# Optimization experiments

Hardware: AMD Instinct MI355X
Metric: run time of the kernel (lower is better)

## Reference

```python
import jax, jax.numpy as jnp
import numpy as np

B, S, H = 4, 2048, 768
NUM_POS = B * (S // 4)  # fixed count of positive clc_label entries (2048, even)
NEG_BIG = -1000000000.0


def setup_inputs() -> dict:
    key = jax.random.key(0)
    k1, k2, k3, k4, k5 = jax.random.split(key, 5)
    encoded_states = jax.random.normal(k1, (B, S, H), dtype=jnp.float32)
    # sorted cell-ids -> contiguous segments for the equality mask
    indicator = jnp.sort(jax.random.randint(k2, (B, S), 0, 256, dtype=jnp.int32), axis=-1)
    # clc_label: first S//4 positions per row are positive targets (class ids in [1,S)),
    # last S//2 positions are -1 (attendable keys), rest 0 (ignored)
    pos_labels = jax.random.randint(k3, (B, S // 4), 1, S, dtype=jnp.int32)
    clc_label = jnp.zeros((B, S), dtype=jnp.int32)
    clc_label = clc_label.at[:, : S // 4].set(pos_labels)
    clc_label = clc_label.at[:, S // 2:].set(-1)
    # uniform_linear params (torch Linear: y = x @ W.T + b)
    W = jax.random.normal(k4, (H, H), dtype=jnp.float32) / np.sqrt(H)
    b = jax.random.normal(k5, (H,), dtype=jnp.float32) * 0.01
    return {"encoded_states": encoded_states, "W": W, "b": b,
            "indicator": indicator, "clc_label": clc_label}


def _ce(logits, labels):
    # mean cross entropy; all labels are > 0 here so ignore_index=0 never triggers
    logp = jax.nn.log_softmax(logits, axis=-1)
    return -jnp.take_along_axis(logp, labels[:, None], axis=1).mean()


def reference(encoded_states, W, b, indicator, clc_label):
    # indicator-equality mask matmul == within-segment sum (the segment-reduce emulation)
    seg_mask = (indicator[:, :, None] == indicator[:, None, :]).astype(encoded_states.dtype)  # [B,S,S]
    agg = jnp.einsum("bij,bjh->bih", seg_mask, encoded_states)  # [B,S,H]
    # Q and K use the SAME linear on the same input -> compute once
    proj = jnp.tanh(agg @ W.T + b)  # [B,S,H]
    scores = jnp.einsum("bih,bjh->bij", proj, proj)  # [B,S,S]
    # attend only to positions where clc_label < 0
    allow = (clc_label < 0)[:, None, :]  # [B,1,S]
    scores = scores + jnp.where(allow, 0.0, NEG_BIG).astype(scores.dtype)
    flat = scores.reshape(-1, S)          # [B*S, S]
    labels = clc_label.reshape(-1)        # [B*S]
    pos_idx = jnp.nonzero(labels > 0, size=NUM_POS)[0]  # row-major order == torch bool-indexing
    logits = flat[pos_idx]                # [NUM_POS, S]
    labs = labels[pos_idx]                # [NUM_POS]
    sep_logits, sep_labels = logits[0::2], labs[0::2]
    tok_logits, tok_labels = logits[1::2], labs[1::2]
    sep_loss = _ce(sep_logits, sep_labels)
    tok_loss = _ce(tok_logits, tok_labels)
    sep_correct = jnp.sum((jnp.argmax(sep_logits, axis=-1).astype(jnp.int32) == sep_labels).astype(jnp.float32))
    tok_correct = jnp.sum((jnp.argmax(tok_logits, axis=-1).astype(jnp.int32) == tok_labels).astype(jnp.float32))
    sep_count = jnp.asarray(sep_logits.shape[0] + 1e-6, dtype=jnp.float32)
    tok_count = jnp.asarray(tok_logits.shape[0] + 1e-6, dtype=jnp.float32)
    return ((sep_loss, sep_correct, sep_count), (tok_loss, tok_correct, tok_count))
```

## Files before the change

kernel.cpp:

```cpp
#include <hip/hip_runtime.h>
#include <math.h>
#include <limits.h>

#define BB 4
#define SS 2048
#define HH 768
#define MAXSEG 256
#define NUM_POS (BB*(SS/4))
#define NEG_BIG -1000000000.0f

typedef _Float16 f16x8 __attribute__((ext_vector_type(8)));
typedef _Float16 f16x4 __attribute__((ext_vector_type(4)));
typedef float    f32x4 __attribute__((ext_vector_type(4)));

__global__ __launch_bounds__(256) void k_scanW(
    const int* __restrict__ ind, const int* __restrict__ clc,
    const float* __restrict__ W, _Float16* __restrict__ Wh,
    int* __restrict__ seg_id, int* __restrict__ seg_start,
    int* __restrict__ nseg, int* __restrict__ pos_local, int* __restrict__ pos_cnt,
    int* __restrict__ allowCnt, int* __restrict__ firstAllow)
{
  int t = threadIdx.x;
  if (blockIdx.x >= BB) {
    int idx = (blockIdx.x - BB)*256 + t;
    float4 v = ((const float4*)W)[idx];
    f16x4 h;
    h[0] = (_Float16)v.x; h[1] = (_Float16)v.y;
    h[2] = (_Float16)v.z; h[3] = (_Float16)v.w;
    *(f16x4*)(Wh + (size_t)idx*4) = h;
    return;
  }
  int b = blockIdx.x;
  int lane = t & 63, wid = t >> 6;
  __shared__ int sInd[SS];
  __shared__ int sWave[4];
  __shared__ int sAC[MAXSEG];
  __shared__ int sFA[MAXSEG];
  for (int i = t; i < SS; i += 256) sInd[i] = ind[b*SS + i];
  sAC[t] = 0; sFA[t] = INT_MAX;
  __syncthreads();

  int i0 = t * 8;
  int f[8], cv[8];
  int lsum = 0;
  #pragma unroll
  for (int u = 0; u < 8; u++) {
    int i = i0 + u;
    f[u] = (i == 0) ? 0 : (sInd[i] != sInd[i-1]);
    cv[u] = clc[b*SS + i];
    lsum += f[u];
  }
  int x = lsum;
  #pragma unroll
  for (int off = 1; off < 64; off <<= 1) {
    int v = __shfl_up(x, off, 64);
    if (lane >= off) x += v;
  }
  if (lane == 63) sWave[wid] = x;
  __syncthreads();
  int base = 0;
  for (int w = 0; w < wid; w++) base += sWave[w];
  int run = base + x - lsum;
  int rid[8];
  #pragma unroll
  for (int u = 0; u < 8; u++) {
    int i = i0 + u;
    run += f[u];
    rid[u] = run;
    seg_id[b*SS + i] = run;
    if (f[u] || i == 0) seg_start[b*(MAXSEG+1) + run] = i;
  }
  if (t == 255) { nseg[b] = run + 1; seg_start[b*(MAXSEG+1) + run + 1] = SS; }

  #pragma unroll
  for (int u = 0; u < 8; u++) {
    if (cv[u] < 0) {
      atomicAdd(&sAC[rid[u]], 1);
      atomicMin(&sFA[rid[u]], i0 + u);
    }
  }
  __syncthreads();
  allowCnt[b*MAXSEG + t]   = sAC[t];
  firstAllow[b*MAXSEG + t] = sFA[t];

  int psum = 0;
  int p[8];
  #pragma unroll
  for (int u = 0; u < 8; u++) { p[u] = (cv[u] > 0) ? 1 : 0; psum += p[u]; }
  x = psum;
  #pragma unroll
  for (int off = 1; off < 64; off <<= 1) {
    int v = __shfl_up(x, off, 64);
    if (lane >= off) x += v;
  }
  __syncthreads();
  if (lane == 63) sWave[wid] = x;
  __syncthreads();
  base = 0;
  for (int w = 0; w < wid; w++) base += sWave[w];
  int rank = base + x - psum;
  #pragma unroll
  for (int u = 0; u < 8; u++) {
    if (p[u]) { pos_local[b*SS + rank] = i0 + u; rank++; }
  }
  if (t == 255) pos_cnt[b] = rank;
}

__global__ __launch_bounds__(256) void k_segsum(
    const float* __restrict__ es,
    const int* __restrict__ seg_start, const int* __restrict__ nseg,
    _Float16* __restrict__ segsum_h)
{
  int blk = blockIdx.x, t = threadIdx.x;
  int b = blk >> 8, s = blk & 255;
  _Float16* o = segsum_h + ((size_t)b*MAXSEG + s)*HH;
  if (s >= nseg[b]) {
    o[t] = (_Float16)0.f; o[t+256] = (_Float16)0.f; o[t+512] = (_Float16)0.f;
    return;
  }
  int st = seg_start[b*(MAXSEG+1) + s];
  int en = seg_start[b*(MAXSEG+1) + s + 1];
  const float* base = es + (size_t)b*SS*HH;
  float a0 = 0.f, a1 = 0.f, a2 = 0.f;
  float b0 = 0.f, b1 = 0.f, b2 = 0.f;
  float c0 = 0.f, c1 = 0.f, c2 = 0.f;
  float d0 = 0.f, d1 = 0.f, d2 = 0.f;
  int i = st;
  for (; i + 4 <= en; i += 4) {
    const float* r0 = base + (size_t)i*HH;
    const float* r1 = r0 + HH;
    const float* r2 = r1 + HH;
    const float* r3 = r2 + HH;
    a0 += r0[t]; a1 += r0[t+256]; a2 += r0[t+512];
    b0 += r1[t]; b1 += r1[t+256]; b2 += r1[t+512];
    c0 += r2[t]; c1 += r2[t+256]; c2 += r2[t+512];
    d0 += r3[t]; d1 += r3[t+256]; d2 += r3[t+512];
  }
  for (; i < en; i++) {
    const float* r = base + (size_t)i*HH;
    a0 += r[t]; a1 += r[t+256]; a2 += r[t+512];
  }
  o[t]     = (_Float16)((a0 + b0) + (c0 + d0));
  o[t+256] = (_Float16)((a1 + b1) + (c1 + d1));
  o[t+512] = (_Float16)((a2 + b2) + (c2 + d2));
}

__global__ __launch_bounds__(256) void k_gemmU(
    const _Float16* __restrict__ Ah, const _Float16* __restrict__ Wh,
    const float* __restrict__ bias, _Float16* __restrict__ Uh)
{
  int tid = threadIdx.x;
  int w = tid >> 6, lane = tid & 63;
  int tile = blockIdx.x*4 + w;
  int tm = tile / 24, tn = tile % 24;
  int rb = tm*32, cb = tn*32;
  int m0 = lane & 15, quad = lane >> 4;
  const _Float16* A0 = Ah + (size_t)(rb + m0)*HH + quad*8;
  const _Float16* A1 = A0 + (size_t)16*HH;
  const _Float16* B0 = Wh + (size_t)(cb + m0)*HH + quad*8;
  const _Float16* B1 = B0 + (size_t)16*HH;
  f32x4 acc00 = {0.f,0.f,0.f,0.f}, acc01 = {0.f,0.f,0.f,0.f};
  f32x4 acc10 = {0.f,0.f,0.f,0.f}, acc11 = {0.f,0.f,0.f,0.f};
  #pragma unroll 4
  for (int k0 = 0; k0 < HH; k0 += 32) {
    f16x8 a0 = *(const f16x8*)(A0 + k0);
    f16x8 a1 = *(const f16x8*)(A1 + k0);
    f16x8 b0 = *(const f16x8*)(B0 + k0);
    f16x8 b1 = *(const f16x8*)(B1 + k0);
    acc00 = __builtin_amdgcn_mfma_f32_16x16x32_f16(a0, b0, acc00, 0, 0, 0);
    acc01 = __builtin_amdgcn_mfma_f32_16x16x32_f16(a0, b1, acc01, 0, 0, 0);
    acc10 = __builtin_amdgcn_mfma_f32_16x16x32_f16(a1, b0, acc10, 0, 0, 0);
    acc11 = __builtin_amdgcn_mfma_f32_16x16x32_f16(a1, b1, acc11, 0, 0, 0);
  }
  float bc0 = bias[cb + m0], bc1 = bias[cb + 16 + m0];
  int r0 = rb + quad*4;
  #pragma unroll
  for (int i = 0; i < 4; i++) {
    Uh[(size_t)(r0+i)*HH    + cb + m0]      = (_Float16)tanhf(acc00[i] + bc0);
    Uh[(size_t)(r0+i)*HH    + cb + 16 + m0] = (_Float16)tanhf(acc01[i] + bc1);
    Uh[(size_t)(r0+16+i)*HH + cb + m0]      = (_Float16)tanhf(acc10[i] + bc0);
    Uh[(size_t)(r0+16+i)*HH + cb + 16 + m0] = (_Float16)tanhf(acc11[i] + bc1);
  }
}

__global__ __launch_bounds__(256) void k_gramlse(
    const _Float16* __restrict__ Uh, const int* __restrict__ allowCnt,
    const int* __restrict__ firstAllow, const int* __restrict__ nseg,
    float* __restrict__ G, float* __restrict__ lse, int* __restrict__ amax)
{
  __shared__ float sG[16][257];
  int t = threadIdx.x;
  int lane = t & 63, w = t >> 6;
  int blk = blockIdx.x;
  int b = blk >> 4;
  int rb = (blk & 15) * 16;
  int m0 = lane & 15, quad = lane >> 4;
  const _Float16* Ub = Uh + (size_t)b*MAXSEG*HH;
  const _Float16* A0 = Ub + (size_t)(rb + m0)*HH + quad*8;
  int cb0 = w * 64;
  const _Float16* B0 = Ub + (size_t)(cb0      + m0)*HH + quad*8;
  const _Float16* B1 = Ub + (size_t)(cb0 + 16 + m0)*HH + quad*8;
  const _Float16* B2 = Ub + (size_t)(cb0 + 32 + m0)*HH + quad*8;
  const _Float16* B3 = Ub + (size_t)(cb0 + 48 + m0)*HH + quad*8;
  f32x4 acc0 = {0.f,0.f,0.f,0.f}, acc1 = {0.f,0.f,0.f,0.f};
  f32x4 acc2 = {0.f,0.f,0.f,0.f}, acc3 = {0.f,0.f,0.f,0.f};
  #pragma unroll 4
  for (int k0 = 0; k0 < HH; k0 += 32) {
    f16x8 a  = *(const f16x8*)(A0 + k0);
    f16x8 q0 = *(const f16x8*)(B0 + k0);
    f16x8 q1 = *(const f16x8*)(B1 + k0);
    f16x8 q2 = *(const f16x8*)(B2 + k0);
    f16x8 q3 = *(const f16x8*)(B3 + k0);
    acc0 = __builtin_amdgcn_mfma_f32_16x16x32_f16(a, q0, acc0, 0, 0, 0);
    acc1 = __builtin_amdgcn_mfma_f32_16x16x32_f16(a, q1, acc1, 0, 0, 0);
    acc2 = __builtin_amdgcn_mfma_f32_16x16x32_f16(a, q2, acc2, 0, 0, 0);
    acc3 = __builtin_amdgcn_mfma_f32_16x16x32_f16(a, q3, acc3, 0, 0, 0);
  }
  float* Gb = G + (size_t)b*MAXSEG*MAXSEG;
  int r0 = quad*4;
  #pragma unroll
  for (int i = 0; i < 4; i++) {
    int rl = r0 + i;
    sG[rl][cb0      + m0] = acc0[i];
    sG[rl][cb0 + 16 + m0] = acc1[i];
    sG[rl][cb0 + 32 + m0] = acc2[i];
    sG[rl][cb0 + 48 + m0] = acc3[i];
    float* gr = Gb + (size_t)(rb + rl)*MAXSEG;
    gr[cb0      + m0] = acc0[i];
    gr[cb0 + 16 + m0] = acc1[i];
    gr[cb0 + 32 + m0] = acc2[i];
    gr[cb0 + 48 + m0] = acc3[i];
  }
  __syncthreads();

  const int* ac = allowCnt + b*MAXSEG;
  const int* fa = firstAllow + b*MAXSEG;
  int ns = nseg[b];
  #pragma unroll
  for (int j = 0; j < 4; j++) {
    int rl = w*4 + j;
    int si = rb + rl;
    if (si >= ns) continue;
    float gv[4]; int av[4], fv[4];
    #pragma unroll
    for (int q = 0; q < 4; q++) {
      int s = lane + 64*q;
      gv[q] = sG[rl][s]; av[q] = ac[s]; fv[q] = fa[s];
    }
    float m = -INFINITY;
    #pragma unroll
    for (int q = 0; q < 4; q++) if (av[q] > 0) m = fmaxf(m, gv[q]);
    #pragma unroll
    for (int off = 32; off > 0; off >>= 1) m = fmaxf(m, __shfl_xor(m, off, 64));
    float s = 0.f;
    #pragma unroll
    for (int q = 0; q < 4; q++) if (av[q] > 0) s += (float)av[q] * expf(gv[q] - m);
    #pragma unroll
    for (int off = 32; off > 0; off >>= 1) s += __shfl_xor(s, off, 64);
    float bv = -INFINITY; int bi = INT_MAX;
    #pragma unroll
    for (int q = 0; q < 4; q++) {
      if (av[q] > 0 && (gv[q] > bv || (gv[q] == bv && fv[q] < bi))) { bv = gv[q]; bi = fv[q]; }
    }
    #pragma unroll
    for (int off = 32; off > 0; off >>= 1) {
      float ov = __shfl_xor(bv, off, 64);
      int   oi = __shfl_xor(bi, off, 64);
      if (ov > bv || (ov == bv && oi < bi)) { bv = ov; bi = oi; }
    }
    if (lane == 0) {
      lse[b*MAXSEG + si]  = m + logf(s);
      amax[b*MAXSEG + si] = bi;
    }
  }
}

__global__ __launch_bounds__(256) void k_posfinal(
    const float* __restrict__ G, const int* __restrict__ seg_id,
    const int* __restrict__ clc, const int* __restrict__ pos_local,
    const int* __restrict__ pos_cnt, const float* __restrict__ lse,
    const int* __restrict__ amax, float* __restrict__ out)
{
  __shared__ int sBase[BB+1];
  __shared__ float sL0[4], sC0[4], sL1[4], sC1[4];
  int t = threadIdx.x;
  if (t == 0) {
    int acc = 0; sBase[0] = 0;
    for (int b = 0; b < BB; b++) { acc += pos_cnt[b]; sBase[b+1] = acc; }
  }
  __syncthreads();
  int total = sBase[BB];
  if (total > NUM_POS) total = NUM_POS;
  float l0 = 0.f, c0 = 0.f, l1 = 0.f, c1 = 0.f;
  for (int r = t; r < total; r += 256) {
    int b = 0;
    while (b < BB-1 && r >= sBase[b+1]) b++;
    int k = r - sBase[b];
    int i  = pos_local[b*SS + k];
    int si = seg_id[b*SS + i];
    int L  = clc[b*SS + i];
    int sL = seg_id[b*SS + L];
    float vL = G[((size_t)b*MAXSEG + si)*MAXSEG + sL] + (clc[b*SS + L] < 0 ? 0.0f : NEG_BIG);
    float loss = lse[b*MAXSEG + si] - vL;
    float corr = (amax[b*MAXSEG + si] == L) ? 1.0f : 0.0f;
    if (r & 1) { l1 += loss; c1 += corr; } else { l0 += loss; c0 += corr; }
  }
  int lane = t & 63, wid = t >> 6;
  #pragma unroll
  for (int off = 32; off > 0; off >>= 1) {
    l0 += __shfl_down(l0, off, 64);
    c0 += __shfl_down(c0, off, 64);
    l1 += __shfl_down(l1, off, 64);
    c1 += __shfl_down(c1, off, 64);
  }
  if (lane == 0) { sL0[wid] = l0; sC0[wid] = c0; sL1[wid] = l1; sC1[wid] = c1; }
  __syncthreads();
  if (t == 0) {
    float L0 = sL0[0]+sL0[1]+sL0[2]+sL0[3];
    float C0 = sC0[0]+sC0[1]+sC0[2]+sC0[3];
    float L1 = sL1[0]+sL1[1]+sL1[2]+sL1[3];
    float C1 = sC1[0]+sC1[1]+sC1[2]+sC1[3];
    float n = (float)(NUM_POS/2);
    out[0] = L0 / n;
    out[1] = C0;
    out[2] = n + 1e-6f;
    out[3] = L1 / n;
    out[4] = C1;
    out[5] = n + 1e-6f;
  }
}

extern "C" void kernel_launch(void* const* d_in, const int* in_sizes, int n_in,
                              void* d_out, int out_size, void* d_ws, size_t ws_size,
                              hipStream_t stream)
{
  const float* es   = (const float*)d_in[0];
  const float* W    = (const float*)d_in[1];
  const float* bias = (const float*)d_in[2];
  const int*   ind  = (const int*)d_in[3];
  const int*   clc  = (const int*)d_in[4];
  float* out = (float*)d_out;

  char* ws = (char*)d_ws;
  int*   nseg       = (int*)(ws + 0);
  int*   pos_cnt    = (int*)(ws + 256);
  int*   seg_start  = (int*)(ws + 1024);
  int*   seg_id     = (int*)(ws + 8192);
  int*   pos_local  = (int*)(ws + 40960);
  int*   allowCnt   = (int*)(ws + 73728);
  int*   firstAllow = (int*)(ws + 77824);
  float* lse        = (float*)(ws + 81920);
  int*   amax       = (int*)(ws + 86016);
  _Float16* segsum_h = (_Float16*)(ws + 90112);
  _Float16* Wh       = (_Float16*)(ws + 1662976);
  _Float16* Uh       = (_Float16*)(ws + 2842624);
  float*    G        = (float*)(ws + 4415488);

  k_scanW<<<BB + 576, 256, 0, stream>>>(ind, clc, W, Wh, seg_id, seg_start,
                                        nseg, pos_local, pos_cnt, allowCnt, firstAllow);
  k_segsum<<<BB*MAXSEG, 256, 0, stream>>>(es, seg_start, nseg, segsum_h);
  k_gemmU<<<192, 256, 0, stream>>>(segsum_h, Wh, bias, Uh);
  k_gramlse<<<BB*16, 256, 0, stream>>>(Uh, allowCnt, firstAllow, nseg, G, lse, amax);
  k_posfinal<<<1, 256, 0, stream>>>(G, seg_id, clc, pos_local, pos_cnt, lse, amax, out);
}
```

Before: 133.8 us.

## Fuse segment scan into segsum blocks, widen gram blocks, batch posfinal loads

The separate scan/W-convert kernel and the segment-sum kernel become one launch. Each segsum block recomputes the segment boundaries for its batch row in shared memory, which removes one launch and the dependency through global seg_start. The gram/LSE kernel now uses 1024-thread blocks, with one 16x16 MFMA tile and one LSE row per wave, giving more waves over the same 64 blocks. The final kernel issues its dependent gathers unrolled by 8 so the loads can overlap. The cost is that the scan is recomputed 256 times per batch row.

```diff
diff --git a/kernel.cpp b/kernel.cpp
--- a/kernel.cpp
+++ b/kernel.cpp
@@ -13,16 +13,19 @@
 typedef _Float16 f16x4 __attribute__((ext_vector_type(4)));
 typedef float    f32x4 __attribute__((ext_vector_type(4)));
 
-__global__ __launch_bounds__(256) void k_scanW(
+__global__ __launch_bounds__(256) void k_stage1(
+    const float* __restrict__ es, const float* __restrict__ W,
     const int* __restrict__ ind, const int* __restrict__ clc,
-    const float* __restrict__ W, _Float16* __restrict__ Wh,
-    int* __restrict__ seg_id, int* __restrict__ seg_start,
-    int* __restrict__ nseg, int* __restrict__ pos_local, int* __restrict__ pos_cnt,
+    _Float16* __restrict__ Wh, _Float16* __restrict__ segsum_h,
+    int* __restrict__ seg_id, int* __restrict__ nseg,
+    int* __restrict__ pos_local, int* __restrict__ pos_cnt,
     int* __restrict__ allowCnt, int* __restrict__ firstAllow)
 {
   int t = threadIdx.x;
-  if (blockIdx.x >= BB) {
-    int idx = (blockIdx.x - BB)*256 + t;
+  int blk = blockIdx.x;
+
+  if (blk >= BB*MAXSEG + BB) {
+    int idx = (blk - (BB*MAXSEG + BB))*256 + t;
     float4 v = ((const float4*)W)[idx];
     f16x4 h;
     h[0] = (_Float16)v.x; h[1] = (_Float16)v.y;
@@ -30,119 +33,150 @@
     *(f16x4*)(Wh + (size_t)idx*4) = h;
     return;
   }
-  int b = blockIdx.x;
+
   int lane = t & 63, wid = t >> 6;
   __shared__ int sInd[SS];
   __shared__ int sWave[4];
+  __shared__ int sStart[MAXSEG+1];
+  __shared__ int sNs;
   __shared__ int sAC[MAXSEG];
   __shared__ int sFA[MAXSEG];
-  for (int i = t; i < SS; i += 256) sInd[i] = ind[b*SS + i];
-  sAC[t] = 0; sFA[t] = INT_MAX;
-  __syncthreads();
-
-  int i0 = t * 8;
-  int f[8], cv[8];
-  int lsum = 0;
-  #pragma unroll
-  for (int u = 0; u < 8; u++) {
-    int i = i0 + u;
-    f[u] = (i == 0) ? 0 : (sInd[i] != sInd[i-1]);
-    cv[u] = clc[b*SS + i];
-    lsum += f[u];
-  }
-  int x = lsum;
-  #pragma unroll
-  for (int off = 1; off < 64; off <<= 1) {
-    int v = __shfl_up(x, off, 64);
-    if (lane >= off) x += v;
-  }
-  if (lane == 63) sWave[wid] = x;
-  __syncthreads();
-  int base = 0;
-  for (int w = 0; w < wid; w++) base += sWave[w];
-  int run = base + x - lsum;
-  int rid[8];
-  #pragma unroll
-  for (int u = 0; u < 8; u++) {
-    int i = i0 + u;
-    run += f[u];
-    rid[u] = run;
-    seg_id[b*SS + i] = run;
-    if (f[u] || i == 0) seg_start[b*(MAXSEG+1) + run] = i;
-  }
-  if (t == 255) { nseg[b] = run + 1; seg_start[b*(MAXSEG+1) + run + 1] = SS; }
-
-  #pragma unroll
-  for (int u = 0; u < 8; u++) {
-    if (cv[u] < 0) {
-      atomicAdd(&sAC[rid[u]], 1);
-      atomicMin(&sFA[rid[u]], i0 + u);
-    }
-  }
-  __syncthreads();
-  allowCnt[b*MAXSEG + t]   = sAC[t];
-  firstAllow[b*MAXSEG + t] = sFA[t];
-
-  int psum = 0;
-  int p[8];
-  #pragma unroll
-  for (int u = 0; u < 8; u++) { p[u] = (cv[u] > 0) ? 1 : 0; psum += p[u]; }
-  x = psum;
-  #pragma unroll
-  for (int off = 1; off < 64; off <<= 1) {
-    int v = __shfl_up(x, off, 64);
-    if (lane >= off) x += v;
-  }
-  __syncthreads();
-  if (lane == 63) sWave[wid] = x;
-  __syncthreads();
-  base = 0;
-  for (int w = 0; w < wid; w++) base += sWave[w];
-  int rank = base + x - psum;
-  #pragma unroll
-  for (int u = 0; u < 8; u++) {
-    if (p[u]) { pos_local[b*SS + rank] = i0 + u; rank++; }
-  }
-  if (t == 255) pos_cnt[b] = rank;
-}
-
-__global__ __launch_bounds__(256) void k_segsum(
-    const float* __restrict__ es,
-    const int* __restrict__ seg_start, const int* __restrict__ nseg,
-    _Float16* __restrict__ segsum_h)
-{
-  int blk = blockIdx.x, t = threadIdx.x;
-  int b = blk >> 8, s = blk & 255;
-  _Float16* o = segsum_h + ((size_t)b*MAXSEG + s)*HH;
-  if (s >= nseg[b]) {
-    o[t] = (_Float16)0.f; o[t+256] = (_Float16)0.f; o[t+512] = (_Float16)0.f;
+
+  if (blk < BB*MAXSEG) {
+    int b = blk >> 8, s = blk & 255;
+    for (int i = t; i < SS; i += 256) sInd[i] = ind[b*SS + i];
+    __syncthreads();
+
+    int i0 = t * 8;
+    int f[8]; int lsum = 0;
+    #pragma unroll
+    for (int u = 0; u < 8; u++) {
+      int i = i0 + u;
+      f[u] = (i == 0) ? 0 : (sInd[i] != sInd[i-1]);
+      lsum += f[u];
+    }
+    int x = lsum;
+    #pragma unroll
+    for (int off = 1; off < 64; off <<= 1) {
+      int v = __shfl_up(x, off, 64);
+      if (lane >= off) x += v;
+    }
+    if (lane == 63) sWave[wid] = x;
+    __syncthreads();
+    int base = 0;
+    for (int w2 = 0; w2 < wid; w2++) base += sWave[w2];
+    int run = base + x - lsum;
+    #pragma unroll
+    for (int u = 0; u < 8; u++) {
+      int i = i0 + u;
+      run += f[u];
+      if (f[u] || i == 0) sStart[run] = i;
+    }
+    if (t == 255) { sStart[run + 1] = SS; sNs = run + 1; }
+    __syncthreads();
+
+    _Float16* o = segsum_h + ((size_t)b*MAXSEG + s)*HH;
+    if (s >= sNs) {
+      o[t] = (_Float16)0.f; o[t+256] = (_Float16)0.f; o[t+512] = (_Float16)0.f;
+      return;
+    }
+    int st = sStart[s];
+    int en = sStart[s + 1];
+    const float* bp = es + (size_t)b*SS*HH;
+    float a0 = 0.f, a1 = 0.f, a2 = 0.f;
+    float b0 = 0.f, b1 = 0.f, b2 = 0.f;
+    float c0 = 0.f, c1 = 0.f, c2 = 0.f;
+    float d0 = 0.f, d1 = 0.f, d2 = 0.f;
+    int i = st;
+    for (; i + 4 <= en; i += 4) {
+      const float* r0 = bp + (size_t)i*HH;
+      const float* r1 = r0 + HH;
+      const float* r2 = r1 + HH;
+      const float* r3 = r2 + HH;
+      a0 += r0[t]; a1 += r0[t+256]; a2 += r0[t+512];
+      b0 += r1[t]; b1 += r1[t+256]; b2 += r1[t+512];
+      c0 += r2[t]; c1 += r2[t+256]; c2 += r2[t+512];
+      d0 += r3[t]; d1 += r3[t+256]; d2 += r3[t+512];
+    }
+    for (; i < en; i++) {
+      const float* r = bp + (size_t)i*HH;
+      a0 += r[t]; a1 += r[t+256]; a2 += r[t+512];
+    }
+    o[t]     = (_Float16)((a0 + b0) + (c0 + d0));
+    o[t+256] = (_Float16)((a1 + b1) + (c1 + d1));
+    o[t+512] = (_Float16)((a2 + b2) + (c2 + d2));
     return;
   }
-  int st = seg_start[b*(MAXSEG+1) + s];
-  int en = seg_start[b*(MAXSEG+1) + s + 1];
-  const float* base = es + (size_t)b*SS*HH;
-  float a0 = 0.f, a1 = 0.f, a2 = 0.f;
-  float b0 = 0.f, b1 = 0.f, b2 = 0.f;
-  float c0 = 0.f, c1 = 0.f, c2 = 0.f;
-  float d0 = 0.f, d1 = 0.f, d2 = 0.f;
-  int i = st;
-  for (; i + 4 <= en; i += 4) {
-    const float* r0 = base + (size_t)i*HH;
-    const float* r1 = r0 + HH;
-    const float* r2 = r1 + HH;
-    const float* r3 = r2 + HH;
-    a0 += r0[t]; a1 += r0[t+256]; a2 += r0[t+512];
-    b0 += r1[t]; b1 += r1[t+256]; b2 += r1[t+512];
-    c0 += r2[t]; c1 += r2[t+256]; c2 += r2[t+512];
-    d0 += r3[t]; d1 += r3[t+256]; d2 += r3[t+512];
-  }
-  for (; i < en; i++) {
-    const float* r = base + (size_t)i*HH;
-    a0 += r[t]; a1 += r[t+256]; a2 += r[t+512];
-  }
-  o[t]     = (_Float16)((a0 + b0) + (c0 + d0));
-  o[t+256] = (_Float16)((a1 + b1) + (c1 + d1));
-  o[t+512] = (_Float16)((a2 + b2) + (c2 + d2));
+
+  {
+    int b = blk - BB*MAXSEG;
+    for (int i = t; i < SS; i += 256) sInd[i] = ind[b*SS + i];
+    sAC[t] = 0; sFA[t] = INT_MAX;
+    __syncthreads();
+
+    int i0 = t * 8;
+    int f[8], cv[8];
+    int lsum = 0;
+    #pragma unroll
+    for (int u = 0; u < 8; u++) {
+      int i = i0 + u;
+      f[u] = (i == 0) ? 0 : (sInd[i] != sInd[i-1]);
+      cv[u] = clc[b*SS + i];
+      lsum += f[u];
+    }
+    int x = lsum;
+    #pragma unroll
+    for (int off = 1; off < 64; off <<= 1) {
+      int v = __shfl_up(x, off, 64);
+      if (lane >= off) x += v;
+    }
+    if (lane == 63) sWave[wid] = x;
+    __syncthreads();
+    int base = 0;
+    for (int w2 = 0; w2 < wid; w2++) base += sWave[w2];
+    int run = base + x - lsum;
+    int rid[8];
+    #pragma unroll
+    for (int u = 0; u < 8; u++) {
+      run += f[u];
+      rid[u] = run;
+      seg_id[b*SS + i0 + u] = run;
+    }
+    if (t == 255) nseg[b] = run + 1;
+
+    #pragma unroll
+    for (int u = 0; u < 8; u++) {
+      if (cv[u] < 0) {
+        atomicAdd(&sAC[rid[u]], 1);
+        atomicMin(&sFA[rid[u]], i0 + u);
+      }
+    }
+    __syncthreads();
+    allowCnt[b*MAXSEG + t]   = sAC[t];
+    firstAllow[b*MAXSEG + t] = sFA[t];
+
+    int psum = 0;
+    int p[8];
+    #pragma unroll
+    for (int u = 0; u < 8; u++) { p[u] = (cv[u] > 0) ? 1 : 0; psum += p[u]; }
+    x = psum;
+    #pragma unroll
+    for (int off = 1; off < 64; off <<= 1) {
+      int v = __shfl_up(x, off, 64);
+      if (lane >= off) x += v;
+    }
+    __syncthreads();
+    if (lane == 63) sWave[wid] = x;
+    __syncthreads();
+    base = 0;
+    for (int w2 = 0; w2 < wid; w2++) base += sWave[w2];
+    int rank = base + x - psum;
+    #pragma unroll
+    for (int u = 0; u < 8; u++) {
+      if (p[u]) { pos_local[b*SS + rank] = i0 + u; rank++; }
+    }
+    if (t == 255) pos_cnt[b] = rank;
+  }
 }
 
 __global__ __launch_bounds__(256) void k_gemmU(
@@ -183,7 +217,7 @@
   }
 }
 
-__global__ __launch_bounds__(256) void k_gramlse(
+__global__ __launch_bounds__(1024) void k_gramlse(
     const _Float16* __restrict__ Uh, const int* __restrict__ allowCnt,
     const int* __restrict__ firstAllow, const int* __restrict__ nseg,
     float* __restrict__ G, float* __restrict__ lse, int* __restrict__ amax)
@@ -197,81 +231,58 @@
   int m0 = lane & 15, quad = lane >> 4;
   const _Float16* Ub = Uh + (size_t)b*MAXSEG*HH;
   const _Float16* A0 = Ub + (size_t)(rb + m0)*HH + quad*8;
-  int cb0 = w * 64;
-  const _Float16* B0 = Ub + (size_t)(cb0      + m0)*HH + quad*8;
-  const _Float16* B1 = Ub + (size_t)(cb0 + 16 + m0)*HH + quad*8;
-  const _Float16* B2 = Ub + (size_t)(cb0 + 32 + m0)*HH + quad*8;
-  const _Float16* B3 = Ub + (size_t)(cb0 + 48 + m0)*HH + quad*8;
-  f32x4 acc0 = {0.f,0.f,0.f,0.f}, acc1 = {0.f,0.f,0.f,0.f};
-  f32x4 acc2 = {0.f,0.f,0.f,0.f}, acc3 = {0.f,0.f,0.f,0.f};
+  int cb = w * 16;
+  const _Float16* B0 = Ub + (size_t)(cb + m0)*HH + quad*8;
+  f32x4 acc = {0.f,0.f,0.f,0.f};
   #pragma unroll 4
   for (int k0 = 0; k0 < HH; k0 += 32) {
     f16x8 a  = *(const f16x8*)(A0 + k0);
-    f16x8 q0 = *(const f16x8*)(B0 + k0);
-    f16x8 q1 = *(const f16x8*)(B1 + k0);
-    f16x8 q2 = *(const f16x8*)(B2 + k0);
-    f16x8 q3 = *(const f16x8*)(B3 + k0);
-    acc0 = __builtin_amdgcn_mfma_f32_16x16x32_f16(a, q0, acc0, 0, 0, 0);
-    acc1 = __builtin_amdgcn_mfma_f32_16x16x32_f16(a, q1, acc1, 0, 0, 0);
-    acc2 = __builtin_amdgcn_mfma_f32_16x16x32_f16(a, q2, acc2, 0, 0, 0);
-    acc3 = __builtin_amdgcn_mfma_f32_16x16x32_f16(a, q3, acc3, 0, 0, 0);
+    f16x8 bb = *(const f16x8*)(B0 + k0);
+    acc = __builtin_amdgcn_mfma_f32_16x16x32_f16(a, bb, acc, 0, 0, 0);
   }
   float* Gb = G + (size_t)b*MAXSEG*MAXSEG;
   int r0 = quad*4;
   #pragma unroll
   for (int i = 0; i < 4; i++) {
-    int rl = r0 + i;
-    sG[rl][cb0      + m0] = acc0[i];
-    sG[rl][cb0 + 16 + m0] = acc1[i];
-    sG[rl][cb0 + 32 + m0] = acc2[i];
-    sG[rl][cb0 + 48 + m0] = acc3[i];
-    float* gr = Gb + (size_t)(rb + rl)*MAXSEG;
-    gr[cb0      + m0] = acc0[i];
-    gr[cb0 + 16 + m0] = acc1[i];
-    gr[cb0 + 32 + m0] = acc2[i];
-    gr[cb0 + 48 + m0] = acc3[i];
+    sG[r0 + i][cb + m0] = acc[i];
+    Gb[(size_t)(rb + r0 + i)*MAXSEG + cb + m0] = acc[i];
   }
   __syncthreads();
 
+  int si = rb + w;
+  if (si >= nseg[b]) return;
   const int* ac = allowCnt + b*MAXSEG;
   const int* fa = firstAllow + b*MAXSEG;
-  int ns = nseg[b];
-  #pragma unroll
-  for (int j = 0; j < 4; j++) {
-    int rl = w*4 + j;
-    int si = rb + rl;
-    if (si >= ns) continue;
-    float gv[4]; int av[4], fv[4];
-    #pragma unroll
-    for (int q = 0; q < 4; q++) {
-      int s = lane + 64*q;
-      gv[q] = sG[rl][s]; av[q] = ac[s]; fv[q] = fa[s];
-    }
-    float m = -INFINITY;
-    #pragma unroll
-    for (int q = 0; q < 4; q++) if (av[q] > 0) m = fmaxf(m, gv[q]);
-    #pragma unroll
-    for (int off = 32; off > 0; off >>= 1) m = fmaxf(m, __shfl_xor(m, off, 64));
-    float s = 0.f;
-    #pragma unroll
-    for (int q = 0; q < 4; q++) if (av[q] > 0) s += (float)av[q] * expf(gv[q] - m);
-    #pragma unroll
-    for (int off = 32; off > 0; off >>= 1) s += __shfl_xor(s, off, 64);
-    float bv = -INFINITY; int bi = INT_MAX;
-    #pragma unroll
-    for (int q = 0; q < 4; q++) {
-      if (av[q] > 0 && (gv[q] > bv || (gv[q] == bv && fv[q] < bi))) { bv = gv[q]; bi = fv[q]; }
-    }
-    #pragma unroll
-    for (int off = 32; off > 0; off >>= 1) {
-      float ov = __shfl_xor(bv, off, 64);
-      int   oi = __shfl_xor(bi, off, 64);
-      if (ov > bv || (ov == bv && oi < bi)) { bv = ov; bi = oi; }
-    }
-    if (lane == 0) {
-      lse[b*MAXSEG + si]  = m + logf(s);
-      amax[b*MAXSEG + si] = bi;
-    }
+  float gv[4]; int av[4], fv[4];
+  #pragma unroll
+  for (int q = 0; q < 4; q++) {
+    int s = lane + 64*q;
+    gv[q] = sG[w][s]; av[q] = ac[s]; fv[q] = fa[s];
+  }
+  float m = -INFINITY;
+  #pragma unroll
+  for (int q = 0; q < 4; q++) if (av[q] > 0) m = fmaxf(m, gv[q]);
+  #pragma unroll
+  for (int off = 32; off > 0; off >>= 1) m = fmaxf(m, __shfl_xor(m, off, 64));
+  float s = 0.f;
+  #pragma unroll
+  for (int q = 0; q < 4; q++) if (av[q] > 0) s += (float)av[q] * expf(gv[q] - m);
+  #pragma unroll
+  for (int off = 32; off > 0; off >>= 1) s += __shfl_xor(s, off, 64);
+  float bv = -INFINITY; int bi = INT_MAX;
+  #pragma unroll
+  for (int q = 0; q < 4; q++) {
+    if (av[q] > 0 && (gv[q] > bv || (gv[q] == bv && fv[q] < bi))) { bv = gv[q]; bi = fv[q]; }
+  }
+  #pragma unroll
+  for (int off = 32; off > 0; off >>= 1) {
+    float ov = __shfl_xor(bv, off, 64);
+    int   oi = __shfl_xor(bi, off, 64);
+    if (ov > bv || (ov == bv && oi < bi)) { bv = ov; bi = oi; }
+  }
+  if (lane == 0) {
+    lse[b*MAXSEG + si]  = m + logf(s);
+    amax[b*MAXSEG + si] = bi;
   }
 }
 
@@ -291,20 +302,50 @@
   __syncthreads();
   int total = sBase[BB];
   if (total > NUM_POS) total = NUM_POS;
+
+  int rs[8]; bool ok[8]; int bv[8];
+  #pragma unroll
+  for (int u = 0; u < 8; u++) {
+    rs[u] = t + 256*u;
+    ok[u] = rs[u] < total;
+    int b = 0;
+    if (ok[u]) { while (b < BB-1 && rs[u] >= sBase[b+1]) b++; }
+    bv[u] = b;
+  }
+  int iv[8];
+  #pragma unroll
+  for (int u = 0; u < 8; u++)
+    iv[u] = ok[u] ? pos_local[bv[u]*SS + (rs[u] - sBase[bv[u]])] : 0;
+  int Lv[8], sv[8];
+  #pragma unroll
+  for (int u = 0; u < 8; u++) {
+    Lv[u] = ok[u] ? clc[bv[u]*SS + iv[u]] : 0;
+    sv[u] = ok[u] ? seg_id[bv[u]*SS + iv[u]] : 0;
+  }
+  int sLv[8], cLv[8];
+  #pragma unroll
+  for (int u = 0; u < 8; u++) {
+    sLv[u] = ok[u] ? seg_id[bv[u]*SS + Lv[u]] : 0;
+    cLv[u] = ok[u] ? clc[bv[u]*SS + Lv[u]] : 0;
+  }
+  float gv[8], lv[8]; int av[8];
+  #pragma unroll
+  for (int u = 0; u < 8; u++) {
+    gv[u] = ok[u] ? G[((size_t)bv[u]*MAXSEG + sv[u])*MAXSEG + sLv[u]] : 0.f;
+    lv[u] = ok[u] ? lse[bv[u]*MAXSEG + sv[u]] : 0.f;
+    av[u] = ok[u] ? amax[bv[u]*MAXSEG + sv[u]] : -1;
+  }
+
   float l0 = 0.f, c0 = 0.f, l1 = 0.f, c1 = 0.f;
-  for (int r = t; r < total; r += 256) {
-    int b = 0;
-    while (b < BB-1 && r >= sBase[b+1]) b++;
-    int k = r - sBase[b];
-    int i  = pos_local[b*SS + k];
-    int si = seg_id[b*SS + i];
-    int L  = clc[b*SS + i];
-    int sL = seg_id[b*SS + L];
-    float vL = G[((size_t)b*MAXSEG + si)*MAXSEG + sL] + (clc[b*SS + L] < 0 ? 0.0f : NEG_BIG);
-    float loss = lse[b*MAXSEG + si] - vL;
-    float corr = (amax[b*MAXSEG + si] == L) ? 1.0f : 0.0f;
-    if (r & 1) { l1 += loss; c1 += corr; } else { l0 += loss; c0 += corr; }
-  }
+  #pragma unroll
+  for (int u = 0; u < 8; u++) {
+    if (!ok[u]) continue;
+    float vL = gv[u] + (cLv[u] < 0 ? 0.0f : NEG_BIG);
+    float loss = lv[u] - vL;
+    float corr = (av[u] == Lv[u]) ? 1.0f : 0.0f;
+    if (rs[u] & 1) { l1 += loss; c1 += corr; } else { l0 += loss; c0 += corr; }
+  }
+
   int lane = t & 63, wid = t >> 6;
   #pragma unroll
   for (int off = 32; off > 0; off >>= 1) {
@@ -344,7 +385,6 @@
   char* ws = (char*)d_ws;
   int*   nseg       = (int*)(ws + 0);
   int*   pos_cnt    = (int*)(ws + 256);
-  int*   seg_start  = (int*)(ws + 1024);
   int*   seg_id     = (int*)(ws + 8192);
   int*   pos_local  = (int*)(ws + 40960);
   int*   allowCnt   = (int*)(ws + 73728);
@@ -356,10 +396,10 @@
   _Float16* Uh       = (_Float16*)(ws + 2842624);
   float*    G        = (float*)(ws + 4415488);
 
-  k_scanW<<<BB + 576, 256, 0, stream>>>(ind, clc, W, Wh, seg_id, seg_start,
-                                        nseg, pos_local, pos_cnt, allowCnt, firstAllow);
-  k_segsum<<<BB*MAXSEG, 256, 0, stream>>>(es, seg_start, nseg, segsum_h);
+  k_stage1<<<BB*MAXSEG + BB + 576, 256, 0, stream>>>(
+      es, W, ind, clc, Wh, segsum_h, seg_id, nseg,
+      pos_local, pos_cnt, allowCnt, firstAllow);
   k_gemmU<<<192, 256, 0, stream>>>(segsum_h, Wh, bias, Uh);
-  k_gramlse<<<BB*16, 256, 0, stream>>>(Uh, allowCnt, firstAllow, nseg, G, lse, amax);
+  k_gramlse<<<BB*16, 1024, 0, stream>>>(Uh, allowCnt, firstAllow, nseg, G, lse, amax);
   k_posfinal<<<1, 256, 0, stream>>>(G, seg_id, clc, pos_local, pos_cnt, lse, amax, out);
 }
```

Result: no change. 133.5 us (-0.2%).
